# Performance work log

Hardware: AMD Instinct MI355X
Metric: run time of the kernel (lower is better)

The kernel has to match this reference:

```python
import jax, jax.numpy as jnp
import numpy as np

# ---- geometry / config constants (from init_kwargs: MandoFanBeamConfig) ----
DET = 816          # detEltCount == sgmWidth
VIEWS = 720        # sgmHeight == views
DU = 1.0           # detEltSize [mm]
OFF = 0.0          # detOffCenter [mm]
SID = 750.0        # source-isocenter distance [mm]
SDD = 1250.0       # source-detector distance [mm]
IMG = 512          # imgDim
PIX = 0.5          # pixelSize [mm]
TOTAL = 2.0 * np.pi  # totalScanAngle = 360 deg
START = 0.0        # startAngle


def make_ramp_filter(N, du):
    # zxInitRampFilter: discrete ramp (Ram-Lak) kernel, center at N//2 - 1
    n = np.arange(N)
    center = N // 2 - 1
    d = n - center
    f = np.zeros(N, dtype=np.float32)
    odd = (d % 2) != 0
    f[odd] = -1.0 / (np.pi * d[odd] * du) ** 2
    f[center] = 1.0 / (2.0 * du) ** 2
    return f


def setup_inputs() -> dict:
    key = jax.random.key(0)
    x = jax.random.normal(key, (8, VIEWS, DET), dtype=jnp.float32)
    filt = jnp.asarray(make_ramp_filter(DET, DU))
    return {"x": x, "filt": filt}


def _filter_sinogram(x, filt):
    # zxFilterSinogram: per-row conv1d with padding='same', then * du.
    # Vectorized: fold (B, H) into the conv batch dim instead of a python loop.
    B, H, W = x.shape
    k = filt.shape[0]
    lhs = x.reshape(B * H, 1, W)                 # (N, C=1, W)
    rhs = filt.reshape(1, 1, k)                  # (O=1, I=1, K) cross-correlation, like torch
    pad = ((k - 1) // 2, k // 2)                 # torch 'same' asymmetric padding for even k
    y = jax.lax.conv_general_dilated(lhs, rhs, window_strides=(1,), padding=[pad])
    return y.reshape(B, H, W) * DU


def _backproject(sgm):
    # Fan-beam FBP backprojection, flat detector, equivalent math to the
    # torch_mando_cuda.backward kernel with KERNEL_NONE (filtering already done).
    B = sgm.shape[0]
    dbeta = TOTAL / VIEWS
    betas = START + jnp.arange(VIEWS, dtype=jnp.float32) * dbeta

    c = (jnp.arange(IMG, dtype=jnp.float32) - (IMG - 1) / 2.0) * PIX
    X, Y = jnp.meshgrid(c, -c)                   # (IMG, IMG); image y axis points up

    # cosine pre-weighting of the (filtered) sinogram: sid / sqrt(sid^2 + u^2)
    u_det = (jnp.arange(DET, dtype=jnp.float32) - (DET - 1) / 2.0) * DU + OFF
    cosw = SID / jnp.sqrt(SID * SID + u_det * u_det)
    sgm_w = sgm * cosw                           # (B, VIEWS, DET)

    def body(img, inp):
        beta, row = inp                          # row: (B, DET)
        cb, sb = jnp.cos(beta), jnp.sin(beta)
        xr = X * cb + Y * sb                     # pixel coords in rotated frame
        yr = -X * sb + Y * cb
        L = SID - yr                             # source-to-pixel distance along central ray
        u = SDD * xr / L                         # detector coordinate hit by this pixel's ray
        w = (SID * SID) / (L * L)                # fan-beam distance weight
        t = (u - OFF) / DU + (DET - 1) / 2.0     # fractional detector index
        i0 = jnp.clip(jnp.floor(t).astype(jnp.int32), 0, DET - 2)
        frac = t - i0.astype(jnp.float32)
        v0 = row[:, i0]                          # (B, IMG, IMG) gather
        v1 = row[:, i0 + 1]
        val = v0 * (1.0 - frac) + v1 * frac      # linear interpolation
        inside = (t >= 0.0) & (t <= DET - 1)
        img = img + jnp.where(inside, w * val, 0.0)
        return img, None

    init = jnp.zeros((B, IMG, IMG), dtype=sgm.dtype)
    img, _ = jax.lax.scan(body, init, (betas, jnp.swapaxes(sgm_w, 0, 1)))
    return img * dbeta


def reference(x, filt):
    x = _filter_sinogram(x, filt)
    return _backproject(x)
```

## Files before the change

### kernel.cpp

```cpp
#include <hip/hip_runtime.h>
#include <math.h>

namespace {
constexpr int DETN = 816;
constexpr int NVIEW = 720;
constexpr int NB = 8;
constexpr int IMGN = 512;
constexpr float PIXSZ = 0.5f;
constexpr float SID = 750.0f;
constexpr float SDD = 1250.0f;
constexpr float DBETA = 6.28318530717958647692f / 720.0f;

constexpr int XPAD2 = 1648;
constexpr int T = 16;
constexpr int TPR = DETN / T;
constexpr int ROWSTRIDE = 1852;
constexpr int NBB = 4;

constexpr int NSPLIT = 2;
constexpr int VH = NVIEW / NSPLIT;
constexpr int VP = VH / 2;
constexpr int VQ = VH / 4;

typedef _Float16 h2 __attribute__((ext_vector_type(2)));
typedef float f2 __attribute__((ext_vector_type(2)));

__device__ __forceinline__ int F(int i) { return i + 2 * (i >> 4); }
__device__ __forceinline__ int pairF(int pp) { return 2 * pp + 2 * (pp >> 3); }

__device__ __forceinline__ f2 fma2(f2 a, f2 b, f2 c) {
  return __builtin_elementwise_fma(a, b, c);
}
__device__ __forceinline__ h2 pack_h2(float a, float b) {
  return __builtin_bit_cast(h2, __builtin_amdgcn_cvt_pkrtz(a, b));
}

__global__ __launch_bounds__(256) void filt_kernel(
    const float* __restrict__ x, const float* __restrict__ filt,
    h2* __restrict__ sino2)
{
  __shared__ float xs[NBB * ROWSTRIDE];
  const int tid = threadIdx.x;
  const int v = blockIdx.x >> 1;
  const int bhalf = blockIdx.x & 1;

  for (int b = 0; b < NBB; ++b) {
    const float* __restrict__ src = &x[((bhalf * NBB + b) * NVIEW + v) * DETN];
    for (int qq = tid; qq < XPAD2; qq += 256) {
      const int s = qq - 407;
      float val = 0.0f;
      if (s >= 0 && s < DETN) val = src[s];
      xs[b * ROWSTRIDE + F(qq)] = val;
    }
  }
  __syncthreads();

  const bool active = tid < NBB * TPR;
  const int b = tid / TPR;
  const int t = tid - b * TPR;
  const int w0 = t * T;
  f2 acc2[8];

  if (active) {
    const float* __restrict__ xrow = &xs[b * ROWSTRIDE];
    const int P0 = 8 * t;
    f2 q16[16];
#pragma unroll
    for (int k = 0; k < 16; ++k)
      q16[k] = *(const f2*)&xrow[pairF(P0 + k)];
#pragma unroll
    for (int k = 0; k < 8; ++k) acc2[k] = (f2){0.0f, 0.0f};

    for (int g = 0; g < 26; ++g) {
#pragma unroll
      for (int u = 0; u < 8; ++u) {
        const int s = 16 * g + u;
        const float fv = filt[2 * s];
        const f2 fv2 = {fv, fv};
#pragma unroll
        for (int k = 0; k < 8; ++k)
          acc2[k] = fma2(q16[(u + k) & 15], fv2, acc2[k]);
        q16[u] = *(const f2*)&xrow[pairF(P0 + s + 16)];
      }
      if (g == 25) break;
#pragma unroll
      for (int u = 0; u < 8; ++u) {
        const int s = 16 * g + 8 + u;
        const float fv = filt[2 * s];
        const f2 fv2 = {fv, fv};
#pragma unroll
        for (int k = 0; k < 8; ++k)
          acc2[k] = fma2(q16[(8 + u + k) & 15], fv2, acc2[k]);
        q16[8 + u] = *(const f2*)&xrow[pairF(P0 + s + 16)];
      }
    }
    const float fc = filt[407];
#pragma unroll
    for (int k = 0; k < 8; ++k) {
      acc2[k].x = fmaf(xrow[F(w0 + 2 * k + 407)], fc, acc2[k].x);
      acc2[k].y = fmaf(xrow[F(w0 + 2 * k + 408)], fc, acc2[k].y);
    }
#pragma unroll
    for (int k = 0; k < 8; ++k) {
      const float udx = (float)(w0 + 2 * k) - 407.5f;
      const float udy = (float)(w0 + 2 * k + 1) - 407.5f;
      acc2[k].x *= SID / sqrtf(SID * SID + udx * udx);
      acc2[k].y *= SID / sqrtf(SID * SID + udy * udy);
    }
  }
  __syncthreads();

  float* ys = xs;
  if (active) {
#pragma unroll
    for (int k = 0; k < 8; ++k) {
      ys[b * (DETN + 1) + w0 + 2 * k] = acc2[k].x;
      ys[b * (DETN + 1) + w0 + 2 * k + 1] = acc2[k].y;
    }
    if (t == 0) ys[b * (DETN + 1) + DETN] = 0.0f;
  }
  __syncthreads();

  h2* dst = sino2 + (size_t)v * DETN * NB + bhalf * NBB;
  for (int idx = tid; idx < DETN * NBB; idx += 256) {
    const int w = idx >> 2;
    const int bb = idx & 3;
    h2 hp;
    hp[0] = (_Float16)ys[bb * (DETN + 1) + w];
    hp[1] = (_Float16)ys[bb * (DETN + 1) + w + 1];
    dst[w * 8 + bb] = hp;
  }
}

__device__ __forceinline__ float dot2acc(h2 w, unsigned int q, float acc) {
  return __builtin_amdgcn_fdot2(w, __builtin_bit_cast(h2, q), acc, false);
}

__global__ __launch_bounds__(256, 6) void bp_kernel(
    const h2* __restrict__ sino2, float* __restrict__ out)
{
  __shared__ f2 cbp_t[VP], sbp_t[VP], csp_t[VP], ssp_t[VP];
  const int tid = threadIdx.x;
  const int v0 = blockIdx.z * VH;
  for (int it = tid; it < VP; it += 256) {
    float sA, cA, sB, cB;
    sincosf((float)(v0 + 2 * it) * DBETA, &sA, &cA);
    sincosf((float)(v0 + 2 * it + 1) * DBETA, &sB, &cB);
    cbp_t[it] = (f2){cA, cB};
    sbp_t[it] = (f2){sA, sB};
    csp_t[it] = (f2){SDD * cA, SDD * cB};
    ssp_t[it] = (f2){SDD * sA, SDD * sB};
  }
  __syncthreads();

  const int lane = tid & 63;
  const int wv = tid >> 6;
  const int px = ((wv & 1) << 3) | (lane & 7);
  const int py = ((wv >> 1) << 3) | (lane >> 3);
  const int j = (blockIdx.x << 4) + px;
  const int i = (blockIdx.y << 4) + py;
  const float X = ((float)j - 255.5f) * PIXSZ;
  const float Y = -(((float)i - 255.5f) * PIXSZ);
  const f2 X2 = {X, X};
  const f2 Y2 = {Y, Y};
  const f2 nY2 = {-Y, -Y};
  const f2 SID2 = {SID, SID};
  const f2 C4075 = {407.5f, 407.5f};

  float acc[NB];
#pragma unroll
  for (int b = 0; b < NB; ++b) acc[b] = 0.0f;

  const char* pv = (const char*)sino2 + (size_t)v0 * DETN * NB * 4;
  constexpr int VSTRIDE = DETN * NB * 4;

  for (int qd = 0; qd < VQ; ++qd) {
    const f2 cb0 = cbp_t[2 * qd],     cb1 = cbp_t[2 * qd + 1];
    const f2 sb0 = sbp_t[2 * qd],     sb1 = sbp_t[2 * qd + 1];
    const f2 cs0 = csp_t[2 * qd],     cs1 = csp_t[2 * qd + 1];
    const f2 ss0 = ssp_t[2 * qd],     ss1 = ssp_t[2 * qd + 1];

    const f2 num0 = fma2(Y2, ss0, X2 * cs0);
    const f2 num1 = fma2(Y2, ss1, X2 * cs1);
    const f2 L0 = fma2(nY2, cb0, fma2(X2, sb0, SID2));
    const f2 L1 = fma2(nY2, cb1, fma2(X2, sb1, SID2));
    const f2 rL0 = {__builtin_amdgcn_rcpf(L0.x), __builtin_amdgcn_rcpf(L0.y)};
    const f2 rL1 = {__builtin_amdgcn_rcpf(L1.x), __builtin_amdgcn_rcpf(L1.y)};
    const f2 tt0 = fma2(num0, rL0, C4075);
    const f2 tt1 = fma2(num1, rL1, C4075);
    const f2 m0 = SID2 * rL0, m1 = SID2 * rL1;
    const f2 w0 = m0 * m0, w1 = m1 * m1;
    const float iA = floorf(tt0.x), iB = floorf(tt0.y);
    const float iC = floorf(tt1.x), iD = floorf(tt1.y);
    const int i0A = (int)iA, i0B = (int)iB, i0C = (int)iC, i0D = (int)iD;
    const f2 fr0 = tt0 - (f2){iA, iB};
    const f2 fr1 = tt1 - (f2){iC, iD};
    const f2 a1p0 = w0 * fr0, a1p1 = w1 * fr1;
    const f2 a0p0 = w0 - a1p0, a0p1 = w1 - a1p1;
    const h2 wpA = pack_h2(a0p0.x, a1p0.x);
    const h2 wpB = pack_h2(a0p0.y, a1p0.y);
    const h2 wpC = pack_h2(a0p1.x, a1p1.x);
    const h2 wpD = pack_h2(a0p1.y, a1p1.y);

    const uint4* pA = (const uint4*)(pv + (i0A << 5));
    const uint4* pB = (const uint4*)(pv + VSTRIDE + (i0B << 5));
    const uint4* pC = (const uint4*)(pv + 2 * VSTRIDE + (i0C << 5));
    const uint4* pD = (const uint4*)(pv + 3 * VSTRIDE + (i0D << 5));
    const uint4 qA0 = pA[0], qA1 = pA[1];
    const uint4 qB0 = pB[0], qB1 = pB[1];
    const uint4 qC0 = pC[0], qC1 = pC[1];
    const uint4 qD0 = pD[0], qD1 = pD[1];

    acc[0] = dot2acc(wpA, qA0.x, acc[0]);
    acc[1] = dot2acc(wpA, qA0.y, acc[1]);
    acc[2] = dot2acc(wpA, qA0.z, acc[2]);
    acc[3] = dot2acc(wpA, qA0.w, acc[3]);
    acc[4] = dot2acc(wpA, qA1.x, acc[4]);
    acc[5] = dot2acc(wpA, qA1.y, acc[5]);
    acc[6] = dot2acc(wpA, qA1.z, acc[6]);
    acc[7] = dot2acc(wpA, qA1.w, acc[7]);

    acc[0] = dot2acc(wpB, qB0.x, acc[0]);
    acc[1] = dot2acc(wpB, qB0.y, acc[1]);
    acc[2] = dot2acc(wpB, qB0.z, acc[2]);
    acc[3] = dot2acc(wpB, qB0.w, acc[3]);
    acc[4] = dot2acc(wpB, qB1.x, acc[4]);
    acc[5] = dot2acc(wpB, qB1.y, acc[5]);
    acc[6] = dot2acc(wpB, qB1.z, acc[6]);
    acc[7] = dot2acc(wpB, qB1.w, acc[7]);

    acc[0] = dot2acc(wpC, qC0.x, acc[0]);
    acc[1] = dot2acc(wpC, qC0.y, acc[1]);
    acc[2] = dot2acc(wpC, qC0.z, acc[2]);
    acc[3] = dot2acc(wpC, qC0.w, acc[3]);
    acc[4] = dot2acc(wpC, qC1.x, acc[4]);
    acc[5] = dot2acc(wpC, qC1.y, acc[5]);
    acc[6] = dot2acc(wpC, qC1.z, acc[6]);
    acc[7] = dot2acc(wpC, qC1.w, acc[7]);

    acc[0] = dot2acc(wpD, qD0.x, acc[0]);
    acc[1] = dot2acc(wpD, qD0.y, acc[1]);
    acc[2] = dot2acc(wpD, qD0.z, acc[2]);
    acc[3] = dot2acc(wpD, qD0.w, acc[3]);
    acc[4] = dot2acc(wpD, qD1.x, acc[4]);
    acc[5] = dot2acc(wpD, qD1.y, acc[5]);
    acc[6] = dot2acc(wpD, qD1.z, acc[6]);
    acc[7] = dot2acc(wpD, qD1.w, acc[7]);

    pv += 4 * VSTRIDE;
  }

#pragma unroll
  for (int b = 0; b < NB; ++b)
    atomicAdd(&out[(b * IMGN + i) * IMGN + j], acc[b] * DBETA);
}

}

extern "C" void kernel_launch(void* const* d_in, const int* in_sizes, int n_in,
                              void* d_out, int out_size, void* d_ws, size_t ws_size,
                              hipStream_t stream) {
  const float* x = (const float*)d_in[0];
  const float* filt = (const float*)d_in[1];
  float* out = (float*)d_out;
  h2* sino2 = (h2*)d_ws;

  (void)hipMemsetAsync(out, 0, (size_t)out_size * sizeof(float), stream);
  filt_kernel<<<NVIEW * 2, 256, 0, stream>>>(x, filt, sino2);
  bp_kernel<<<dim3(IMGN / 16, IMGN / 16, NSPLIT), 256, 0, stream>>>(sino2, out);
}
```

Before: 250.2 us.

## Process two adjacent pixels per thread with first-order geometry and shared gathers

Each thread now handles two horizontally adjacent pixels, so the grid is halved in x. The second pixel's reciprocal distance comes from a first-order Taylor update of the first (rL1 ≈ rL0 - 0.5*sin*rL0^2) instead of a second rcp. Its detector sample is reused when both pixels land on the same detector bin, which skips a second gather. Register use rises (two sets of 8 accumulators), so the occupancy hint drops from 6 to 4 waves, and the linearised reciprocal adds a small accuracy error.

Result: slower. 314.3 us (+25.6%).

```diff
diff --git a/kernel.cpp b/kernel.cpp
--- a/kernel.cpp
+++ b/kernel.cpp
@@ -20,7 +20,6 @@
 constexpr int NSPLIT = 2;
 constexpr int VH = NVIEW / NSPLIT;
 constexpr int VP = VH / 2;
-constexpr int VQ = VH / 4;
 
 typedef _Float16 h2 __attribute__((ext_vector_type(2)));
 typedef float f2 __attribute__((ext_vector_type(2)));
@@ -136,7 +135,7 @@
   return __builtin_amdgcn_fdot2(w, __builtin_bit_cast(h2, q), acc, false);
 }
 
-__global__ __launch_bounds__(256, 6) void bp_kernel(
+__global__ __launch_bounds__(256, 4) void bp_kernel(
     const h2* __restrict__ sino2, float* __restrict__ out)
 {
   __shared__ f2 cbp_t[VP], sbp_t[VP], csp_t[VP], ssp_t[VP];
@@ -155,10 +154,8 @@
 
   const int lane = tid & 63;
   const int wv = tid >> 6;
-  const int px = ((wv & 1) << 3) | (lane & 7);
-  const int py = ((wv >> 1) << 3) | (lane >> 3);
-  const int j = (blockIdx.x << 4) + px;
-  const int i = (blockIdx.y << 4) + py;
+  const int j = (blockIdx.x << 5) + ((wv & 1) << 4) + ((lane & 7) << 1);
+  const int i = (blockIdx.y << 4) + ((wv >> 1) << 3) + (lane >> 3);
   const float X = ((float)j - 255.5f) * PIXSZ;
   const float Y = -(((float)i - 255.5f) * PIXSZ);
   const f2 X2 = {X, X};
@@ -166,93 +163,113 @@
   const f2 nY2 = {-Y, -Y};
   const f2 SID2 = {SID, SID};
   const f2 C4075 = {407.5f, 407.5f};
-
-  float acc[NB];
-#pragma unroll
-  for (int b = 0; b < NB; ++b) acc[b] = 0.0f;
+  const f2 HALF2 = {0.5f, 0.5f};
+
+  float acc0[NB], acc1[NB];
+#pragma unroll
+  for (int b = 0; b < NB; ++b) { acc0[b] = 0.0f; acc1[b] = 0.0f; }
 
   const char* pv = (const char*)sino2 + (size_t)v0 * DETN * NB * 4;
   constexpr int VSTRIDE = DETN * NB * 4;
 
-  for (int qd = 0; qd < VQ; ++qd) {
-    const f2 cb0 = cbp_t[2 * qd],     cb1 = cbp_t[2 * qd + 1];
-    const f2 sb0 = sbp_t[2 * qd],     sb1 = sbp_t[2 * qd + 1];
-    const f2 cs0 = csp_t[2 * qd],     cs1 = csp_t[2 * qd + 1];
-    const f2 ss0 = ssp_t[2 * qd],     ss1 = ssp_t[2 * qd + 1];
-
-    const f2 num0 = fma2(Y2, ss0, X2 * cs0);
-    const f2 num1 = fma2(Y2, ss1, X2 * cs1);
-    const f2 L0 = fma2(nY2, cb0, fma2(X2, sb0, SID2));
-    const f2 L1 = fma2(nY2, cb1, fma2(X2, sb1, SID2));
+  for (int it = 0; it < VP; ++it) {
+    const f2 cb2 = cbp_t[it];
+    const f2 sb2 = sbp_t[it];
+    const f2 cs2 = csp_t[it];
+    const f2 ss2 = ssp_t[it];
+
+    const f2 num0 = fma2(Y2, ss2, X2 * cs2);
+    const f2 L0 = fma2(nY2, cb2, fma2(X2, sb2, SID2));
     const f2 rL0 = {__builtin_amdgcn_rcpf(L0.x), __builtin_amdgcn_rcpf(L0.y)};
-    const f2 rL1 = {__builtin_amdgcn_rcpf(L1.x), __builtin_amdgcn_rcpf(L1.y)};
     const f2 tt0 = fma2(num0, rL0, C4075);
+    const f2 m0 = SID2 * rL0;
+    const f2 w0v = m0 * m0;
+    const f2 hcs = HALF2 * cs2;
+    const f2 hsb = HALF2 * sb2;
+    const f2 rL0sq = rL0 * rL0;
+    const f2 rL1 = fma2(-hsb, rL0sq, rL0);
+    const f2 num1 = num0 + hcs;
     const f2 tt1 = fma2(num1, rL1, C4075);
-    const f2 m0 = SID2 * rL0, m1 = SID2 * rL1;
-    const f2 w0 = m0 * m0, w1 = m1 * m1;
-    const float iA = floorf(tt0.x), iB = floorf(tt0.y);
-    const float iC = floorf(tt1.x), iD = floorf(tt1.y);
-    const int i0A = (int)iA, i0B = (int)iB, i0C = (int)iC, i0D = (int)iD;
-    const f2 fr0 = tt0 - (f2){iA, iB};
-    const f2 fr1 = tt1 - (f2){iC, iD};
-    const f2 a1p0 = w0 * fr0, a1p1 = w1 * fr1;
-    const f2 a0p0 = w0 - a1p0, a0p1 = w1 - a1p1;
-    const h2 wpA = pack_h2(a0p0.x, a1p0.x);
-    const h2 wpB = pack_h2(a0p0.y, a1p0.y);
-    const h2 wpC = pack_h2(a0p1.x, a1p1.x);
-    const h2 wpD = pack_h2(a0p1.y, a1p1.y);
-
-    const uint4* pA = (const uint4*)(pv + (i0A << 5));
-    const uint4* pB = (const uint4*)(pv + VSTRIDE + (i0B << 5));
-    const uint4* pC = (const uint4*)(pv + 2 * VSTRIDE + (i0C << 5));
-    const uint4* pD = (const uint4*)(pv + 3 * VSTRIDE + (i0D << 5));
-    const uint4 qA0 = pA[0], qA1 = pA[1];
-    const uint4 qB0 = pB[0], qB1 = pB[1];
-    const uint4 qC0 = pC[0], qC1 = pC[1];
-    const uint4 qD0 = pD[0], qD1 = pD[1];
-
-    acc[0] = dot2acc(wpA, qA0.x, acc[0]);
-    acc[1] = dot2acc(wpA, qA0.y, acc[1]);
-    acc[2] = dot2acc(wpA, qA0.z, acc[2]);
-    acc[3] = dot2acc(wpA, qA0.w, acc[3]);
-    acc[4] = dot2acc(wpA, qA1.x, acc[4]);
-    acc[5] = dot2acc(wpA, qA1.y, acc[5]);
-    acc[6] = dot2acc(wpA, qA1.z, acc[6]);
-    acc[7] = dot2acc(wpA, qA1.w, acc[7]);
-
-    acc[0] = dot2acc(wpB, qB0.x, acc[0]);
-    acc[1] = dot2acc(wpB, qB0.y, acc[1]);
-    acc[2] = dot2acc(wpB, qB0.z, acc[2]);
-    acc[3] = dot2acc(wpB, qB0.w, acc[3]);
-    acc[4] = dot2acc(wpB, qB1.x, acc[4]);
-    acc[5] = dot2acc(wpB, qB1.y, acc[5]);
-    acc[6] = dot2acc(wpB, qB1.z, acc[6]);
-    acc[7] = dot2acc(wpB, qB1.w, acc[7]);
-
-    acc[0] = dot2acc(wpC, qC0.x, acc[0]);
-    acc[1] = dot2acc(wpC, qC0.y, acc[1]);
-    acc[2] = dot2acc(wpC, qC0.z, acc[2]);
-    acc[3] = dot2acc(wpC, qC0.w, acc[3]);
-    acc[4] = dot2acc(wpC, qC1.x, acc[4]);
-    acc[5] = dot2acc(wpC, qC1.y, acc[5]);
-    acc[6] = dot2acc(wpC, qC1.z, acc[6]);
-    acc[7] = dot2acc(wpC, qC1.w, acc[7]);
-
-    acc[0] = dot2acc(wpD, qD0.x, acc[0]);
-    acc[1] = dot2acc(wpD, qD0.y, acc[1]);
-    acc[2] = dot2acc(wpD, qD0.z, acc[2]);
-    acc[3] = dot2acc(wpD, qD0.w, acc[3]);
-    acc[4] = dot2acc(wpD, qD1.x, acc[4]);
-    acc[5] = dot2acc(wpD, qD1.y, acc[5]);
-    acc[6] = dot2acc(wpD, qD1.z, acc[6]);
-    acc[7] = dot2acc(wpD, qD1.w, acc[7]);
-
-    pv += 4 * VSTRIDE;
-  }
-
-#pragma unroll
-  for (int b = 0; b < NB; ++b)
-    atomicAdd(&out[(b * IMGN + i) * IMGN + j], acc[b] * DBETA);
+    const f2 m1 = SID2 * rL1;
+    const f2 w1v = m1 * m1;
+
+    {
+      const int rA = __float2int_rd(tt0.x);
+      const float frA = tt0.x - (float)rA;
+      const float a1A = w0v.x * frA;
+      const h2 wA = pack_h2(w0v.x - a1A, a1A);
+      const int rB = __float2int_rd(tt1.x);
+      const float frB = tt1.x - (float)rB;
+      const float a1B = w1v.x * frB;
+      const h2 wB = pack_h2(w1v.x - a1B, a1B);
+
+      const uint4* pa = (const uint4*)(pv + (rA << 5));
+      const uint4 qa0 = pa[0], qa1 = pa[1];
+      uint4 qb0 = qa0, qb1 = qa1;
+      if (rB != rA) {
+        const uint4* pb = (const uint4*)(pv + (rB << 5));
+        qb0 = pb[0]; qb1 = pb[1];
+      }
+      acc0[0] = dot2acc(wA, qa0.x, acc0[0]);
+      acc0[1] = dot2acc(wA, qa0.y, acc0[1]);
+      acc0[2] = dot2acc(wA, qa0.z, acc0[2]);
+      acc0[3] = dot2acc(wA, qa0.w, acc0[3]);
+      acc0[4] = dot2acc(wA, qa1.x, acc0[4]);
+      acc0[5] = dot2acc(wA, qa1.y, acc0[5]);
+      acc0[6] = dot2acc(wA, qa1.z, acc0[6]);
+      acc0[7] = dot2acc(wA, qa1.w, acc0[7]);
+      acc1[0] = dot2acc(wB, qb0.x, acc1[0]);
+      acc1[1] = dot2acc(wB, qb0.y, acc1[1]);
+      acc1[2] = dot2acc(wB, qb0.z, acc1[2]);
+      acc1[3] = dot2acc(wB, qb0.w, acc1[3]);
+      acc1[4] = dot2acc(wB, qb1.x, acc1[4]);
+      acc1[5] = dot2acc(wB, qb1.y, acc1[5]);
+      acc1[6] = dot2acc(wB, qb1.z, acc1[6]);
+      acc1[7] = dot2acc(wB, qb1.w, acc1[7]);
+    }
+    {
+      const int rA = __float2int_rd(tt0.y);
+      const float frA = tt0.y - (float)rA;
+      const float a1A = w0v.y * frA;
+      const h2 wA = pack_h2(w0v.y - a1A, a1A);
+      const int rB = __float2int_rd(tt1.y);
+      const float frB = tt1.y - (float)rB;
+      const float a1B = w1v.y * frB;
+      const h2 wB = pack_h2(w1v.y - a1B, a1B);
+
+      const uint4* pa = (const uint4*)(pv + VSTRIDE + (rA << 5));
+      const uint4 qa0 = pa[0], qa1 = pa[1];
+      uint4 qb0 = qa0, qb1 = qa1;
+      if (rB != rA) {
+        const uint4* pb = (const uint4*)(pv + VSTRIDE + (rB << 5));
+        qb0 = pb[0]; qb1 = pb[1];
+      }
+      acc0[0] = dot2acc(wA, qa0.x, acc0[0]);
+      acc0[1] = dot2acc(wA, qa0.y, acc0[1]);
+      acc0[2] = dot2acc(wA, qa0.z, acc0[2]);
+      acc0[3] = dot2acc(wA, qa0.w, acc0[3]);
+      acc0[4] = dot2acc(wA, qa1.x, acc0[4]);
+      acc0[5] = dot2acc(wA, qa1.y, acc0[5]);
+      acc0[6] = dot2acc(wA, qa1.z, acc0[6]);
+      acc0[7] = dot2acc(wA, qa1.w, acc0[7]);
+      acc1[0] = dot2acc(wB, qb0.x, acc1[0]);
+      acc1[1] = dot2acc(wB, qb0.y, acc1[1]);
+      acc1[2] = dot2acc(wB, qb0.z, acc1[2]);
+      acc1[3] = dot2acc(wB, qb0.w, acc1[3]);
+      acc1[4] = dot2acc(wB, qb1.x, acc1[4]);
+      acc1[5] = dot2acc(wB, qb1.y, acc1[5]);
+      acc1[6] = dot2acc(wB, qb1.z, acc1[6]);
+      acc1[7] = dot2acc(wB, qb1.w, acc1[7]);
+    }
+
+    pv += 2 * VSTRIDE;
+  }
+
+#pragma unroll
+  for (int b = 0; b < NB; ++b) {
+    atomicAdd(&out[(b * IMGN + i) * IMGN + j], acc0[b] * DBETA);
+    atomicAdd(&out[(b * IMGN + i) * IMGN + j + 1], acc1[b] * DBETA);
+  }
 }
 
 }
@@ -267,5 +284,5 @@
 
   (void)hipMemsetAsync(out, 0, (size_t)out_size * sizeof(float), stream);
   filt_kernel<<<NVIEW * 2, 256, 0, stream>>>(x, filt, sino2);
-  bp_kernel<<<dim3(IMGN / 16, IMGN / 16, NSPLIT), 256, 0, stream>>>(sino2, out);
-}
+  bp_kernel<<<dim3(IMGN / 32, IMGN / 16, NSPLIT), 256, 0, stream>>>(sino2, out);
+}
```
